# Kernel optimization log

Measured on AMD Instinct MI355X. Metric: run time of the kernel, lower is better.

The kernel has to match this reference:

```python
import jax, jax.numpy as jnp
import numpy as np

B, D_IN, LAT, C = 16384, 512, 64, 8
HID = [1024, 512, 256]

def _lin(k, fi, fo, scale=0.02):
    k1, k2 = jax.random.split(k)
    return jax.random.normal(k1, (fi, fo), jnp.float32) * scale, jax.random.normal(k2, (fo,), jnp.float32) * scale

def _lin_c(k, fi, fo, scale=0.02):
    k1, k2 = jax.random.split(k)
    return jax.random.normal(k1, (C, fi, fo), jnp.float32) * scale, jax.random.normal(k2, (C, fo), jnp.float32) * scale

def setup_inputs() -> dict:
    key = jax.random.key(0)
    ks = jax.random.split(key, 16)
    x = jax.random.normal(ks[0], (B, D_IN), jnp.float32)
    cluster_labels = jax.random.randint(ks[1], (B,), 0, C, jnp.int32)
    eps = jax.random.normal(ks[2], (B, LAT), jnp.float32)
    # encoder: shared(512->1024), unshared(1024->512), shared(512->256)
    enc_W0, enc_b0 = _lin(ks[3], D_IN, HID[0])
    enc_Wu, enc_bu = _lin_c(ks[4], HID[0], HID[1])
    enc_W2, enc_b2 = _lin(ks[5], HID[1], HID[2])
    # shared latent heads
    mu_W, mu_b = _lin(ks[6], HID[2], LAT)
    lv_W, lv_b = _lin(ks[7], HID[2], LAT)
    # decoder (hidden_dims reversed = [256,512,1024]): unshared(64->256), shared(256->512), unshared(512->1024)
    dec_Wu0, dec_bu0 = _lin_c(ks[8], LAT, HID[2])
    dec_W1, dec_b1 = _lin(ks[9], HID[2], HID[1])
    dec_Wu2, dec_bu2 = _lin_c(ks[10], HID[1], HID[0])
    # per-cluster final layer (1024 -> input_dim), no activation (all-continuous)
    fin_W, fin_b = _lin_c(ks[11], HID[0], D_IN)
    return dict(x=x, cluster_labels=cluster_labels, eps=eps,
                enc_W0=enc_W0, enc_b0=enc_b0, enc_Wu=enc_Wu, enc_bu=enc_bu,
                enc_W2=enc_W2, enc_b2=enc_b2, mu_W=mu_W, mu_b=mu_b,
                lv_W=lv_W, lv_b=lv_b, dec_Wu0=dec_Wu0, dec_bu0=dec_bu0,
                dec_W1=dec_W1, dec_b1=dec_b1, dec_Wu2=dec_Wu2, dec_bu2=dec_bu2,
                fin_W=fin_W, fin_b=fin_b)

def _unshared(h, W, b, labels):
    # per-cluster GEMM then row-wise combine (mask-based dispatch, no row reorder)
    y = jnp.einsum('bi,cio->bco', h, W) + b[None]  # [B, C, out]
    return jnp.take_along_axis(y, labels[:, None, None], axis=1)[:, 0, :]

def reference(x, cluster_labels, eps,
              enc_W0, enc_b0, enc_Wu, enc_bu, enc_W2, enc_b2,
              mu_W, mu_b, lv_W, lv_b,
              dec_Wu0, dec_bu0, dec_W1, dec_b1, dec_Wu2, dec_bu2,
              fin_W, fin_b):
    lbl = cluster_labels.astype(jnp.int32)
    # encoder
    h = jax.nn.relu(x @ enc_W0 + enc_b0)
    h = jax.nn.relu(_unshared(h, enc_Wu, enc_bu, lbl))
    h = jax.nn.relu(h @ enc_W2 + enc_b2)
    mu = h @ mu_W + mu_b
    logvar = h @ lv_W + lv_b
    # reparameterize
    z = mu + jnp.exp(0.5 * logvar) * eps
    # decoder
    h = jax.nn.relu(_unshared(z, dec_Wu0, dec_bu0, lbl))
    h = jax.nn.relu(h @ dec_W1 + dec_b1)
    h = jax.nn.relu(_unshared(h, dec_Wu2, dec_bu2, lbl))
    # per-cluster final output layer (identity activation: all-continuous)
    recon = _unshared(h, fin_W, fin_b, lbl)
    return recon
```

## Files before the change

### kernel.cpp

```cpp
#include <hip/hip_runtime.h>

typedef _Float16 f16;
typedef __attribute__((ext_vector_type(8))) _Float16 f16x8;
typedef __attribute__((ext_vector_type(4))) _Float16 f16x4;
typedef __attribute__((ext_vector_type(4))) float    f32x4;

#define B_ROWS 16384
#define MPAD   17408
#define MTILES 136
#define NBLK   64

typedef __attribute__((address_space(1))) void as1_void;
typedef __attribute__((address_space(3))) void as3_void;

__device__ __forceinline__ void gl_lds16(const void* g, void* l) {
    __builtin_amdgcn_global_load_lds((const as1_void*)g, (as3_void*)l, 16, 0, 0);
}


__global__ __launch_bounds__(256) void k_prep(const int* __restrict__ lbl, int* __restrict__ blockhist,
                                              int* __restrict__ rowmap,
                                              const float* __restrict__ mb_, const float* __restrict__ lb_,
                                              float* __restrict__ bz, f16* __restrict__ zerob) {
    int b = blockIdx.x, t = threadIdx.x;
    int i = b * 256 + t;
    rowmap[i] = -1;
    if (b < NBLK) {
        __shared__ int h[8];
        if (t < 8) h[t] = 0;
        __syncthreads();
        atomicAdd(&h[lbl[i]], 1);
        __syncthreads();
        if (t < 8) blockhist[b * 8 + t] = h[t];
    } else if (b == NBLK) {
        if (t < 64) zerob[t] = (f16)0.f;
        if (t < 64) bz[t] = mb_[t];
        else if (t < 128) bz[t] = lb_[t - 64];
    }
}

__global__ void k_offsets(const int* __restrict__ blockhist, int* offs, int* tilec, int* blockbase) {
    __shared__ int tot[8];
    __shared__ int so[9];
    int t = threadIdx.x;
    if (t < 8) {
        int s = 0;
        for (int b = 0; b < NBLK; ++b) s += blockhist[b * 8 + t];
        tot[t] = s;
    }
    __syncthreads();
    if (t == 0) {
        int o = 0;
        for (int c = 0; c < 8; ++c) { so[c] = o; o += (tot[c] + 127) & ~127; }
        so[8] = o;
        for (int c = 0; c < 9; ++c) offs[c] = so[c];
    }
    __syncthreads();
    if (t < 8) {
        int run = so[t];
        for (int b = 0; b < NBLK; ++b) {
            blockbase[b * 8 + t] = run;
            run += blockhist[b * 8 + t];
        }
    }
    if (t < MTILES) {
        int row = t * 128, c = 7;
        for (int cc = 0; cc < 8; ++cc)
            if (row >= so[cc] && row < so[cc + 1]) c = cc;
        tilec[t] = c;
    }
}

__global__ __launch_bounds__(256) void k_scatter(const int* __restrict__ lbl,
                                                 const int* __restrict__ blockbase,
                                                 int* __restrict__ rowmap) {
    __shared__ int cur[8];
    if (threadIdx.x < 8) cur[threadIdx.x] = blockbase[blockIdx.x * 8 + threadIdx.x];
    __syncthreads();
    int i = blockIdx.x * 256 + threadIdx.x;
    int c = lbl[i];
    int pos = atomicAdd(&cur[c], 1);
    rowmap[pos] = i;
}


struct Seg { const float* s; f16* d; int K, N, b0, nx, ny; long sCS, dCS; };
struct SegTab { Seg g[10]; };

__global__ __launch_bounds__(256) void k_trans(SegTab tab, const float* __restrict__ x, f16* __restrict__ xh) {
    int bid = blockIdx.x;
    if (bid < tab.g[1].b0) {
        int i = bid * 256 + threadIdx.x;
        float4 v = ((const float4*)x)[i];
        f16x4 o = {(f16)v.x, (f16)v.y, (f16)v.z, (f16)v.w};
        ((f16x4*)xh)[i] = o;
        return;
    }
    int s = 9;
    while (bid < tab.g[s].b0) --s;
    Seg sg = tab.g[s];
    int lb = bid - sg.b0;
    int nxy = sg.nx * sg.ny;
    int z = lb / nxy; int r = lb - z * nxy;
    int by = r / sg.nx; int bx = r - by * sg.nx;
    const float* src = sg.s + (size_t)z * sg.sCS;
    f16* dst = sg.d + (size_t)z * sg.dCS;
    int n0 = bx * 32, k0 = by * 32;
    int tx = threadIdx.x & 31, ty = threadIdx.x >> 5;
    __shared__ float t[32][33];
    #pragma unroll
    for (int i = 0; i < 32; i += 8)
        t[ty + i][tx] = src[(size_t)(k0 + ty + i) * sg.N + n0 + tx];
    __syncthreads();
    #pragma unroll
    for (int i = 0; i < 32; i += 8)
        dst[(size_t)(n0 + ty + i) * sg.K + k0 + tx] = (f16)t[tx][ty + i];
}


template<int GATHER, int PERW, int RELU, int EPI>
__global__ __launch_bounds__(256) void gemm_k(
    const f16* __restrict__ A, const f16* __restrict__ Wt,
    const float* __restrict__ bias, f16* __restrict__ Out, float* __restrict__ OutF,
    const float* __restrict__ eps,
    const int* __restrict__ rowmap, const int* __restrict__ tilec,
    const f16* __restrict__ zerobuf, int K, int N)
{
    __shared__ __align__(16) char smem[32768];
    char* lA = smem;
    char* lB = smem + 16384;
    const int tid  = threadIdx.x;
    const int wave = tid >> 6;
    const int lane = tid & 63;

    const int id  = blockIdx.x;
    const int xcd = id & 7;
    const int jj  = id >> 3;
    const int tm  = (jj % 17) * 8 + xcd;
    const int tn  = jj / 17;
    const int r0 = tm * 128, n0 = tn * 128;

    const f16* wb = Wt;
    const float* bb = bias;
    if (PERW) {
        int c = tilec[tm];
        wb += (size_t)c * K * N;
        bb += (size_t)c * N;
    }

    const int srow = tid >> 3;
    const int sg   = tid & 7;
    const int xk16 = (sg ^ (srow & 7)) * 16;
    const size_t rowB = (size_t)K * 2;
    const size_t passB = 32 * rowB;

    const char* pa[4]; size_t stepA[4];
    #pragma unroll
    for (int p = 0; p < 4; ++p) {
        int gr = r0 + p * 32 + srow;
        if (GATHER) {
            int g = rowmap[gr];
            if (g >= 0) { pa[p] = (const char*)(A + (size_t)g * K) + xk16; stepA[p] = 128; }
            else        { pa[p] = (const char*)zerobuf;                    stepA[p] = 0;   }
        } else {
            pa[p] = (const char*)(A + (size_t)gr * K) + xk16; stepA[p] = 128;
        }
    }
    const char* pb = (const char*)(wb + (size_t)(n0 + srow) * K) + xk16;

    const int mb = (wave >> 1) * 64;
    const int nb = (wave & 1) * 64;
    const int quad = lane >> 4;
    const int r16  = lane & 15;
    const int key  = r16 & 7;

    f32x4 acc[4][4];
    #pragma unroll
    for (int i = 0; i < 4; ++i)
        #pragma unroll
        for (int j = 0; j < 4; ++j)
            acc[i][j] = (f32x4){0.f, 0.f, 0.f, 0.f};

    const int nk = K >> 6;
    for (int kb = 0; kb < nk; ++kb) {
        #pragma unroll
        for (int p = 0; p < 4; ++p)
            gl_lds16(pa[p], lA + p * 4096 + wave * 1024);
        #pragma unroll
        for (int p = 0; p < 4; ++p)
            gl_lds16(pb + p * passB, lB + p * 4096 + wave * 1024);
        __syncthreads();
        #pragma unroll
        for (int kk = 0; kk < 2; ++kk) {
            const int off = ((kk * 4 + quad) ^ key) * 16;
            f16x8 af[4], bf[4];
            #pragma unroll
            for (int i = 0; i < 4; ++i)
                af[i] = *(const f16x8*)(lA + (mb + i * 16 + r16) * 128 + off);
            #pragma unroll
            for (int j = 0; j < 4; ++j)
                bf[j] = *(const f16x8*)(lB + (nb + j * 16 + r16) * 128 + off);
            #pragma unroll
            for (int i = 0; i < 4; ++i)
                #pragma unroll
                for (int j = 0; j < 4; ++j)
                    acc[i][j] = __builtin_amdgcn_mfma_f32_16x16x32_f16(af[i], bf[j], acc[i][j], 0, 0, 0);
        }
        __syncthreads();
        #pragma unroll
        for (int p = 0; p < 4; ++p) pa[p] += stepA[p];
        pb += 128;
    }

    float bv[4];
    #pragma unroll
    for (int j = 0; j < 4; ++j) bv[j] = bb[n0 + nb + j * 16 + r16];

    if (EPI == 1) {
        #pragma unroll
        for (int p = 0; p < 2; ++p) {
            if ((mb >> 6) == p) {
                #pragma unroll
                for (int i = 0; i < 4; ++i) {
                    #pragma unroll
                    for (int r = 0; r < 4; ++r) {
                        int lr2 = i * 16 + quad * 4 + r;
                        #pragma unroll
                        for (int j = 0; j < 4; ++j) {
                            int lc = nb + j * 16 + r16;
                            float v = acc[i][j][r] + bv[j];
                            if (RELU) v = fmaxf(v, 0.f);
                            *(float*)(smem + lr2 * 512 + ((((lc >> 2) ^ (lr2 & 7))) << 4) + ((lc & 3) << 2)) = v;
                        }
                    }
                }
            }
            __syncthreads();
            #pragma unroll
            for (int k = 0; k < 8; ++k) {
                int f = k * 256 + tid;
                int row2 = f >> 5, g5 = f & 31;
                int grow = rowmap[r0 + p * 64 + row2];
                f32x4 vv = *(const f32x4*)(smem + row2 * 512 + (((g5 ^ (row2 & 7))) << 4));
                if (grow >= 0)
                    *(f32x4*)(OutF + (size_t)grow * N + n0 + g5 * 4) = vv;
            }
            __syncthreads();
        }
        return;
    }

    #pragma unroll
    for (int i = 0; i < 4; ++i) {
        #pragma unroll
        for (int r = 0; r < 4; ++r) {
            int lr = mb + i * 16 + quad * 4 + r;
            #pragma unroll
            for (int j = 0; j < 4; ++j) {
                int lc = nb + j * 16 + r16;
                float v = acc[i][j][r] + bv[j];
                if (RELU) v = fmaxf(v, 0.f);
                *(f16*)(smem + lr * 256 + ((((lc >> 3) ^ (lr & 7))) << 4) + ((lc & 7) << 1)) = (f16)v;
            }
        }
    }
    __syncthreads();

    if (EPI == 0) {
        #pragma unroll
        for (int k = 0; k < 8; ++k) {
            int f = k * 256 + tid;
            int row = f >> 4, g4 = f & 15;
            f16x8 vv = *(const f16x8*)(smem + row * 256 + (((g4 ^ (row & 7))) << 4));
            *(f16x8*)(Out + (size_t)(r0 + row) * N + n0 + g4 * 8) = vv;
        }
    } else {
        const int col = tid & 63;
        const int rb  = tid >> 6;
        for (int rr = 0; rr < 32; ++rr) {
            int row = rb * 32 + rr;
            int g = rowmap[r0 + row];
            float e = (g >= 0) ? eps[(size_t)g * 64 + col] : 0.f;
            float mu = (float)*(const f16*)(smem + row * 256 + ((((col >> 3) ^ (row & 7))) << 4) + ((col & 7) << 1));
            int c2 = col + 64;
            float lv = (float)*(const f16*)(smem + row * 256 + ((((c2 >> 3) ^ (row & 7))) << 4) + ((c2 & 7) << 1));
            Out[(size_t)(r0 + row) * 64 + col] = (f16)(mu + expf(0.5f * lv) * e);
        }
    }
}


extern "C" void kernel_launch(void* const* d_in, const int* in_sizes, int n_in,
                              void* d_out, int out_size, void* d_ws, size_t ws_size,
                              hipStream_t stream) {
    const float* x      = (const float*)d_in[0];
    const int*   lbl    = (const int*)  d_in[1];
    const float* eps    = (const float*)d_in[2];
    const float* enc_W0 = (const float*)d_in[3];
    const float* enc_b0 = (const float*)d_in[4];
    const float* enc_Wu = (const float*)d_in[5];
    const float* enc_bu = (const float*)d_in[6];
    const float* enc_W2 = (const float*)d_in[7];
    const float* enc_b2 = (const float*)d_in[8];
    const float* mu_W   = (const float*)d_in[9];
    const float* mu_b   = (const float*)d_in[10];
    const float* lv_W   = (const float*)d_in[11];
    const float* lv_b   = (const float*)d_in[12];
    const float* dWu0   = (const float*)d_in[13];
    const float* dbu0   = (const float*)d_in[14];
    const float* dW1    = (const float*)d_in[15];
    const float* db1    = (const float*)d_in[16];
    const float* dWu2   = (const float*)d_in[17];
    const float* dbu2   = (const float*)d_in[18];
    const float* finW   = (const float*)d_in[19];
    const float* finb   = (const float*)d_in[20];
    float* out = (float*)d_out;
    (void)in_sizes; (void)n_in; (void)out_size; (void)ws_size;

    char* base = (char*)d_ws;
    size_t off = 0;
    auto alloc = [&](size_t bytes) { char* r = base + off; off = (off + bytes + 255) & ~(size_t)255; return r; };
    f16* xh     = (f16*)alloc((size_t)B_ROWS * 512 * 2);
    f16* buf1   = (f16*)alloc((size_t)MPAD * 1024 * 2);
    f16* buf2   = (f16*)alloc((size_t)MPAD * 512 * 2);
    f16* buf3   = (f16*)alloc((size_t)MPAD * 256 * 2);
    f16* zb     = (f16*)alloc((size_t)MPAD * 64 * 2);
    f16* w0t    = (f16*)alloc(1024ul * 512 * 2);
    f16* wut    = (f16*)alloc(8ul * 512 * 1024 * 2);
    f16* w2t    = (f16*)alloc(256ul * 512 * 2);
    f16* wzt    = (f16*)alloc(128ul * 256 * 2);
    f16* wd0t   = (f16*)alloc(8ul * 256 * 64 * 2);
    f16* wd1t   = (f16*)alloc(512ul * 256 * 2);
    f16* wd2t   = (f16*)alloc(8ul * 1024 * 512 * 2);
    f16* wft    = (f16*)alloc(8ul * 512 * 1024 * 2);
    float* bz   = (float*)alloc(128 * 4);
    int* rowmap = (int*)alloc(MPAD * 4);
    int* blockhist = (int*)alloc(NBLK * 8 * 4);
    int* blockbase = (int*)alloc(NBLK * 8 * 4);
    int* offs   = (int*)alloc(64);
    int* tilec  = (int*)alloc(MTILES * 4);
    f16* zerob  = (f16*)alloc(256);

    k_prep<<<MPAD / 256, 256, 0, stream>>>(lbl, blockhist, rowmap, mu_b, lv_b, bz, zerob);
    k_offsets<<<1, 256, 0, stream>>>(blockhist, offs, tilec, blockbase);
    k_scatter<<<NBLK, 256, 0, stream>>>(lbl, blockbase, rowmap);

    SegTab tab;
    int b0 = B_ROWS * 512 / 4 / 256;
    auto seg = [&](int i, const float* s, f16* d, int K, int N, int nz, long sCS, long dCS) {
        int nx = N / 32, ny = K / 32;
        tab.g[i] = Seg{s, d, K, N, b0, nx, ny, sCS, dCS};
        b0 += nx * ny * nz;
    };
    tab.g[0] = Seg{nullptr, nullptr, 0, 0, 0, 0, 0, 0, 0};
    seg(1, enc_W0, w0t, 512, 1024, 1, 0, 0);
    seg(2, enc_Wu, wut, 1024, 512, 8, 1024l * 512, 512l * 1024);
    seg(3, enc_W2, w2t, 512, 256, 1, 0, 0);
    seg(4, mu_W, wzt, 256, 64, 1, 0, 0);
    seg(5, lv_W, wzt + 64 * 256, 256, 64, 1, 0, 0);
    seg(6, dWu0, wd0t, 64, 256, 8, 64l * 256, 256l * 64);
    seg(7, dW1, wd1t, 256, 512, 1, 0, 0);
    seg(8, dWu2, wd2t, 512, 1024, 8, 512l * 1024, 1024l * 512);
    seg(9, finW, wft, 1024, 512, 8, 1024l * 512, 512l * 1024);
    k_trans<<<b0, 256, 0, stream>>>(tab, x, xh);

    gemm_k<1,0,1,0><<<MTILES * 8, 256, 0, stream>>>(xh,   w0t,  enc_b0, buf1, nullptr, nullptr, rowmap, tilec, zerob, 512, 1024);
    gemm_k<0,1,1,0><<<MTILES * 4, 256, 0, stream>>>(buf1, wut,  enc_bu, buf2, nullptr, nullptr, rowmap, tilec, zerob, 1024, 512);
    gemm_k<0,0,1,0><<<MTILES * 2, 256, 0, stream>>>(buf2, w2t,  enc_b2, buf3, nullptr, nullptr, rowmap, tilec, zerob, 512, 256);
    gemm_k<0,0,0,2><<<MTILES * 1, 256, 0, stream>>>(buf3, wzt,  bz,     zb,   nullptr, eps,     rowmap, tilec, zerob, 256, 128);
    gemm_k<0,1,1,0><<<MTILES * 2, 256, 0, stream>>>(zb,   wd0t, dbu0,   buf3, nullptr, nullptr, rowmap, tilec, zerob, 64, 256);
    gemm_k<0,0,1,0><<<MTILES * 4, 256, 0, stream>>>(buf3, wd1t, db1,    buf2, nullptr, nullptr, rowmap, tilec, zerob, 256, 512);
    gemm_k<0,1,1,0><<<MTILES * 8, 256, 0, stream>>>(buf2, wd2t, dbu2,   buf1, nullptr, nullptr, rowmap, tilec, zerob, 512, 1024);
    gemm_k<0,1,0,1><<<MTILES * 4, 256, 0, stream>>>(buf1, wft,  finb,   nullptr, out,  nullptr, rowmap, tilec, zerob, 1024, 512);
}
```

Baseline: 384.2 us.

## Double-buffer GEMM LDS tiles and write epilogue directly from registers

Doubles shared memory to 64KB and ping-pongs between two stages, issuing global->LDS loads for the next K block before computing the current one, so each K step needs one barrier instead of two and loads overlap the MFMAs. The EPI 0/1 epilogues now store straight from accumulators to global memory instead of staging through LDS for coalesced vector writes. The larger LDS footprint may lower occupancy. The direct scalar stores are less coalesced, especially the fp32 scatter to OutF.

```diff
diff --git a/kernel.cpp b/kernel.cpp
--- a/kernel.cpp
+++ b/kernel.cpp
@@ -126,9 +126,7 @@
     const int* __restrict__ rowmap, const int* __restrict__ tilec,
     const f16* __restrict__ zerobuf, int K, int N)
 {
-    __shared__ __align__(16) char smem[32768];
-    char* lA = smem;
-    char* lB = smem + 16384;
+    __shared__ __align__(16) char smem[65536];
     const int tid  = threadIdx.x;
     const int wave = tid >> 6;
     const int lane = tid & 63;
@@ -174,6 +172,10 @@
     const int r16  = lane & 15;
     const int key  = r16 & 7;
 
+    float bv[4];
+    #pragma unroll
+    for (int j = 0; j < 4; ++j) bv[j] = bb[n0 + nb + j * 16 + r16];
+
     f32x4 acc[4][4];
     #pragma unroll
     for (int i = 0; i < 4; ++i)
@@ -181,15 +183,19 @@
         for (int j = 0; j < 4; ++j)
             acc[i][j] = (f32x4){0.f, 0.f, 0.f, 0.f};
 
-    const int nk = K >> 6;
-    for (int kb = 0; kb < nk; ++kb) {
+    auto stage = [&](char* dst) {
         #pragma unroll
         for (int p = 0; p < 4; ++p)
-            gl_lds16(pa[p], lA + p * 4096 + wave * 1024);
+            gl_lds16(pa[p], dst + p * 4096 + wave * 1024);
         #pragma unroll
         for (int p = 0; p < 4; ++p)
-            gl_lds16(pb + p * passB, lB + p * 4096 + wave * 1024);
-        __syncthreads();
+            gl_lds16(pb + p * passB, dst + 16384 + p * 4096 + wave * 1024);
+        #pragma unroll
+        for (int p = 0; p < 4; ++p) pa[p] += stepA[p];
+        pb += 128;
+    };
+
+    auto compute = [&](const char* lA, const char* lB) {
         #pragma unroll
         for (int kk = 0; kk < 2; ++kk) {
             const int off = ((kk * 4 + quad) ^ key) * 16;
@@ -206,85 +212,68 @@
                 for (int j = 0; j < 4; ++j)
                     acc[i][j] = __builtin_amdgcn_mfma_f32_16x16x32_f16(af[i], bf[j], acc[i][j], 0, 0, 0);
         }
+    };
+
+    const int nk = K >> 6;
+    stage(smem);
+    __syncthreads();
+    int cur = 0;
+    for (int kb = 0; kb < nk - 1; ++kb) {
+        stage(smem + ((cur ^ 1) << 15));
+        compute(smem + (cur << 15), smem + (cur << 15) + 16384);
         __syncthreads();
-        #pragma unroll
-        for (int p = 0; p < 4; ++p) pa[p] += stepA[p];
-        pb += 128;
-    }
-
-    float bv[4];
-    #pragma unroll
-    for (int j = 0; j < 4; ++j) bv[j] = bb[n0 + nb + j * 16 + r16];
-
-    if (EPI == 1) {
-        #pragma unroll
-        for (int p = 0; p < 2; ++p) {
-            if ((mb >> 6) == p) {
+        cur ^= 1;
+    }
+    compute(smem + (cur << 15), smem + (cur << 15) + 16384);
+
+    if (EPI == 2) {
+        char* cs = smem + ((cur ^ 1) << 15);
+        #pragma unroll
+        for (int i = 0; i < 4; ++i) {
+            #pragma unroll
+            for (int r = 0; r < 4; ++r) {
+                int lr = mb + i * 16 + quad * 4 + r;
                 #pragma unroll
-                for (int i = 0; i < 4; ++i) {
-                    #pragma unroll
-                    for (int r = 0; r < 4; ++r) {
-                        int lr2 = i * 16 + quad * 4 + r;
-                        #pragma unroll
-                        for (int j = 0; j < 4; ++j) {
-                            int lc = nb + j * 16 + r16;
-                            float v = acc[i][j][r] + bv[j];
-                            if (RELU) v = fmaxf(v, 0.f);
-                            *(float*)(smem + lr2 * 512 + ((((lc >> 2) ^ (lr2 & 7))) << 4) + ((lc & 3) << 2)) = v;
-                        }
-                    }
+                for (int j = 0; j < 4; ++j) {
+                    int lc = nb + j * 16 + r16;
+                    float v = acc[i][j][r] + bv[j];
+                    *(f16*)(cs + lr * 256 + ((((lc >> 3) ^ (lr & 7))) << 4) + ((lc & 7) << 1)) = (f16)v;
                 }
             }
-            __syncthreads();
-            #pragma unroll
-            for (int k = 0; k < 8; ++k) {
-                int f = k * 256 + tid;
-                int row2 = f >> 5, g5 = f & 31;
-                int grow = rowmap[r0 + p * 64 + row2];
-                f32x4 vv = *(const f32x4*)(smem + row2 * 512 + (((g5 ^ (row2 & 7))) << 4));
-                if (grow >= 0)
-                    *(f32x4*)(OutF + (size_t)grow * N + n0 + g5 * 4) = vv;
-            }
-            __syncthreads();
-        }
-        return;
-    }
-
-    #pragma unroll
-    for (int i = 0; i < 4; ++i) {
-        #pragma unroll
-        for (int r = 0; r < 4; ++r) {
-            int lr = mb + i * 16 + quad * 4 + r;
-            #pragma unroll
-            for (int j = 0; j < 4; ++j) {
-                int lc = nb + j * 16 + r16;
-                float v = acc[i][j][r] + bv[j];
-                if (RELU) v = fmaxf(v, 0.f);
-                *(f16*)(smem + lr * 256 + ((((lc >> 3) ^ (lr & 7))) << 4) + ((lc & 7) << 1)) = (f16)v;
-            }
-        }
-    }
-    __syncthreads();
-
-    if (EPI == 0) {
-        #pragma unroll
-        for (int k = 0; k < 8; ++k) {
-            int f = k * 256 + tid;
-            int row = f >> 4, g4 = f & 15;
-            f16x8 vv = *(const f16x8*)(smem + row * 256 + (((g4 ^ (row & 7))) << 4));
-            *(f16x8*)(Out + (size_t)(r0 + row) * N + n0 + g4 * 8) = vv;
-        }
-    } else {
+        }
+        __syncthreads();
         const int col = tid & 63;
         const int rb  = tid >> 6;
         for (int rr = 0; rr < 32; ++rr) {
             int row = rb * 32 + rr;
             int g = rowmap[r0 + row];
             float e = (g >= 0) ? eps[(size_t)g * 64 + col] : 0.f;
-            float mu = (float)*(const f16*)(smem + row * 256 + ((((col >> 3) ^ (row & 7))) << 4) + ((col & 7) << 1));
+            float mu = (float)*(const f16*)(cs + row * 256 + ((((col >> 3) ^ (row & 7))) << 4) + ((col & 7) << 1));
             int c2 = col + 64;
-            float lv = (float)*(const f16*)(smem + row * 256 + ((((c2 >> 3) ^ (row & 7))) << 4) + ((c2 & 7) << 1));
+            float lv = (float)*(const f16*)(cs + row * 256 + ((((c2 >> 3) ^ (row & 7))) << 4) + ((c2 & 7) << 1));
             Out[(size_t)(r0 + row) * 64 + col] = (f16)(mu + expf(0.5f * lv) * e);
+        }
+        return;
+    }
+
+    #pragma unroll
+    for (int i = 0; i < 4; ++i) {
+        #pragma unroll
+        for (int r = 0; r < 4; ++r) {
+            int orow = r0 + mb + i * 16 + quad * 4 + r;
+            int g = 0;
+            if (EPI == 1) g = rowmap[orow];
+            #pragma unroll
+            for (int j = 0; j < 4; ++j) {
+                int ocol = n0 + nb + j * 16 + r16;
+                float v = acc[i][j][r] + bv[j];
+                if (RELU) v = fmaxf(v, 0.f);
+                if (EPI == 1) {
+                    if (g >= 0) OutF[(size_t)g * N + ocol] = v;
+                } else {
+                    Out[(size_t)orow * N + ocol] = (f16)v;
+                }
+            }
         }
     }
 }
```

After: 362.6 us. 5.6% less time.
